# Performance work log

Measured on AMD Instinct MI355X. Metric: run time of the kernel, lower is better.

The kernel has to match this reference:

```python
import jax, jax.numpy as jnp
import numpy as np

B, C, L = 16, 128, 2048


def setup_inputs() -> dict:
    key = jax.random.key(0)
    ks = jax.random.split(key, 7)
    s = 1.0 / np.sqrt(C)  # torch Conv1d default init scale
    x = jax.random.normal(ks[0], (B, C, L), dtype=jnp.float32)
    W1 = jax.random.uniform(ks[1], (C, C), jnp.float32, -s, s)
    b1 = jax.random.uniform(ks[2], (C,), jnp.float32, -s, s)
    W2 = jax.random.uniform(ks[3], (C, C), jnp.float32, -s, s)
    b2 = jax.random.uniform(ks[4], (C,), jnp.float32, -s, s)
    W3 = jax.random.uniform(ks[5], (C, C), jnp.float32, -s, s)
    b3 = jax.random.uniform(ks[6], (C,), jnp.float32, -s, s)
    return {"x": x, "W1": W1, "b1": b1, "W2": W2, "b2": b2, "W3": W3, "b3": b3}


def _conv1x1(x, W, b):
    # x: [B,C,L], W: [out,in] -> [B,out,L]
    return jnp.einsum('oc,bcl->bol', W, x) + b[None, :, None]


def reference(x, W1, b1, W2, b2, W3, b3):
    q = _conv1x1(x, W1, b1).transpose(0, 2, 1)  # [B,L,C]
    k = _conv1x1(x, W2, b2).transpose(0, 2, 1)  # [B,L,C]
    v = _conv1x1(x, W3, b3).transpose(0, 2, 1)  # [B,L,C]
    attn = jnp.einsum('bic,bjc->bij', q, k)     # [B,L,L]
    attn = jax.nn.softmax(attn, axis=-1)
    out = jnp.einsum('bij,bjc->bic', attn, v)   # [B,L,C]
    return out.transpose(0, 2, 1)               # [B,C,L]
```

## Files before the change

kernel.cpp:

```cpp
#include <hip/hip_runtime.h>
#include <hip/hip_bf16.h>
#include <stdint.h>

#define B_ 16
#define C_ 128
#define L_ 2048
#define LOG2E 1.4426950408889634f

typedef __attribute__((ext_vector_type(8))) short bf16x8;
typedef __attribute__((ext_vector_type(4))) float f32x4;

typedef __attribute__((address_space(3))) unsigned int lds_u32_t;
typedef const __attribute__((address_space(1))) unsigned int gbl_u32_t;

__device__ __forceinline__ void gload_lds16(const void* g, void* l) {
  __builtin_amdgcn_global_load_lds((gbl_u32_t*)g,
                                   (lds_u32_t*)(unsigned long long)l, 16, 0, 0);
}

__device__ __forceinline__ unsigned short f2bf(float x) {
  union { float f; unsigned u; } v; v.f = x;
  unsigned u = v.u;
  u += 0x7fffu + ((u >> 16) & 1u);
  return (unsigned short)(u >> 16);
}

__device__ __forceinline__ unsigned pk2(float a, float b) {
  return (unsigned)f2bf(a) | ((unsigned)f2bf(b) << 16);
}

__global__ __launch_bounds__(256, 2) void proj_kernel(
    const float* __restrict__ x,
    const float* __restrict__ W1, const float* __restrict__ b1,
    const float* __restrict__ W2, const float* __restrict__ b2,
    const float* __restrict__ W3, const float* __restrict__ b3,
    unsigned short* __restrict__ Qo, unsigned short* __restrict__ Ko,
    unsigned short* __restrict__ Vt)
{
  __shared__ unsigned short Xt[64][136];
  __shared__ unsigned short Wl[128][136];

  const int b  = blockIdx.x & 15;
  const int lt = blockIdx.x >> 4;
  const int l0 = lt * 64;
  const int tid = threadIdx.x;
  const int w = tid >> 6, lane = tid & 63, li = lane & 15, lg = lane >> 4;

  for (int it = 0; it < 8; ++it) {
    int idx = tid + it * 256;
    int c = idx >> 4, f4 = idx & 15;
    const float4 vv = *(const float4*)(x + (size_t)(b * C_ + c) * L_ + l0 + f4 * 4);
    Xt[f4 * 4 + 0][c] = f2bf(vv.x);
    Xt[f4 * 4 + 1][c] = f2bf(vv.y);
    Xt[f4 * 4 + 2][c] = f2bf(vv.z);
    Xt[f4 * 4 + 3][c] = f2bf(vv.w);
  }

  auto stageW = [&](const float* W) {
    for (int it = 0; it < 16; ++it) {
      int idx = tid + it * 256;
      int o = idx >> 5, f4 = idx & 31;
      const float4 vv = *(const float4*)(W + (size_t)o * C_ + f4 * 4);
      unsigned short* p = &Wl[o][f4 * 4];
      p[0] = f2bf(vv.x); p[1] = f2bf(vv.y); p[2] = f2bf(vv.z); p[3] = f2bf(vv.w);
    }
  };

  auto computePhase = [&](const float* bias, unsigned short* Out, int mode) {
    f32x4 acc[8];
#pragma unroll
    for (int ni = 0; ni < 8; ++ni) acc[ni] = (f32x4){0.f, 0.f, 0.f, 0.f};
    bf16x8 af[4];
#pragma unroll
    for (int kk = 0; kk < 4; ++kk)
      af[kk] = *(const bf16x8*)&Xt[w * 16 + li][lg * 8 + kk * 32];
#pragma unroll
    for (int kk = 0; kk < 4; ++kk) {
#pragma unroll
      for (int ni = 0; ni < 8; ++ni) {
        bf16x8 bf = *(const bf16x8*)&Wl[ni * 16 + li][lg * 8 + kk * 32];
        acc[ni] = __builtin_amdgcn_mfma_f32_16x16x32_bf16(af[kk], bf, acc[ni], 0, 0, 0);
      }
    }
    if (mode == 0) {
#pragma unroll
      for (int ni = 0; ni < 8; ++ni) {
        float bv = bias[ni * 16 + li];
#pragma unroll
        for (int r = 0; r < 4; ++r) {
          int lrow = l0 + w * 16 + lg * 4 + r;
          Out[(size_t)(b * L_ + lrow) * C_ + ni * 16 + li] = f2bf(acc[ni][r] + bv);
        }
      }
    } else {
#pragma unroll
      for (int ni = 0; ni < 8; ++ni) {
        float bv = bias[ni * 16 + li];
        int o = ni * 16 + li;
        unsigned long long pw =
            (unsigned long long)pk2(acc[ni][0] + bv, acc[ni][1] + bv) |
            ((unsigned long long)pk2(acc[ni][2] + bv, acc[ni][3] + bv) << 32);
        *(unsigned long long*)(Out + (size_t)(b * C_ + o) * L_ + l0 + w * 16 + lg * 4) = pw;
      }
    }
  };

  stageW(W1);
  __syncthreads();
  computePhase(b1, Qo, 0);
  __syncthreads();
  stageW(W2);
  __syncthreads();
  computePhase(b2, Ko, 0);
  __syncthreads();
  stageW(W3);
  __syncthreads();
  computePhase(b3, Vt, 1);
}

__global__ __launch_bounds__(512, 2) void attn_kernel(
    const unsigned short* __restrict__ Q,
    const unsigned short* __restrict__ K,
    const unsigned short* __restrict__ Vt,
    float* __restrict__ out)
{
  __shared__ unsigned short kbuf[2][64 * C_];
  __shared__ unsigned short vbuf[2][C_ * 64];
  __shared__ unsigned short pbuf[8][16 * 64];

  const int b  = blockIdx.x & 15;
  const int qt = blockIdx.x >> 4;
  const int tid = threadIdx.x;
  const int w = tid >> 6, lane = tid & 63, li = lane & 15, lg = lane >> 4;
  const int qrow0 = qt * 128 + w * 16;
  const size_t bLC = (size_t)b * L_ * C_;

  bf16x8 qf[4];
  {
    const unsigned short* qp = Q + bLC + (size_t)(qrow0 + li) * C_ + lg * 8;
#pragma unroll
    for (int kk = 0; kk < 4; ++kk) qf[kk] = *(const bf16x8*)(qp + kk * 32);
  }

  f32x4 oacc[8];
#pragma unroll
  for (int i = 0; i < 8; ++i) oacc[i] = (f32x4){0.f, 0.f, 0.f, 0.f};
  float mrun = -1e30f, lrun = 0.f;

  const char* kgb = (const char*)(K + bLC);
  const char* vgb = (const char*)(Vt + bLC);

  auto stage = [&](int sel, int t) {
    const char* kt  = kgb + (size_t)t * (64 * 256);
    const char* vt0 = vgb + (size_t)t * 128;
    int dbase = w * 2048;
#pragma unroll
    for (int i2 = 0; i2 < 2; ++i2) {
      int db = dbase + i2 * 1024;
      int d  = db + lane * 16;
      int row = d >> 8, cb = d & 255;
      gload_lds16(kt + row * 256 + (cb ^ ((row & 7) << 4)), (char*)kbuf[sel] + db);
      int rowv = d >> 7, cbv = d & 127;
      gload_lds16(vt0 + (size_t)rowv * (L_ * 2) + (cbv ^ ((rowv & 7) << 4)),
                  (char*)vbuf[sel] + db);
    }
  };

  stage(0, 0);
  __syncthreads();

  int cur = 0;
  for (int t = 0; t < 32; ++t) {
    if (t + 1 < 32) stage(cur ^ 1, t + 1);

    const char* kb = (const char*)kbuf[cur];
    bf16x8 kf[4][4];
#pragma unroll
    for (int mt = 0; mt < 4; ++mt) {
      int row = mt * 16 + li;
      int rb = row << 8, swz = (row & 7) << 4;
#pragma unroll
      for (int kk = 0; kk < 4; ++kk)
        kf[mt][kk] = *(const bf16x8*)(kb + rb + ((lg * 16 + kk * 64) ^ swz));
    }
    f32x4 s[4];
#pragma unroll
    for (int mt = 0; mt < 4; ++mt) {
      s[mt] = (f32x4){0.f, 0.f, 0.f, 0.f};
#pragma unroll
      for (int kk = 0; kk < 4; ++kk)
        s[mt] = __builtin_amdgcn_mfma_f32_16x16x32_bf16(kf[mt][kk], qf[kk], s[mt], 0, 0, 0);
    }

    float pmax = -1e30f;
#pragma unroll
    for (int mt = 0; mt < 4; ++mt)
#pragma unroll
      for (int r = 0; r < 4; ++r) pmax = fmaxf(pmax, s[mt][r]);
    pmax = fmaxf(pmax, __shfl_xor(pmax, 16));
    pmax = fmaxf(pmax, __shfl_xor(pmax, 32));
    float mnew  = fmaxf(mrun, pmax);
    float alpha = exp2f((mrun - mnew) * LOG2E);
    float psum = 0.f;
#pragma unroll
    for (int mt = 0; mt < 4; ++mt) {
      float p0 = exp2f((s[mt][0] - mnew) * LOG2E);
      float p1 = exp2f((s[mt][1] - mnew) * LOG2E);
      float p2 = exp2f((s[mt][2] - mnew) * LOG2E);
      float p3 = exp2f((s[mt][3] - mnew) * LOG2E);
      psum += (p0 + p1) + (p2 + p3);
      unsigned long long pw = (unsigned long long)pk2(p0, p1) |
                              ((unsigned long long)pk2(p2, p3) << 32);
      int cb = mt * 32 + lg * 8;
      *(unsigned long long*)((char*)pbuf[w] + li * 128 + (cb ^ ((li & 7) << 4))) = pw;
    }
    psum += __shfl_xor(psum, 16);
    psum += __shfl_xor(psum, 32);
    lrun = lrun * alpha + psum;
#pragma unroll
    for (int ct = 0; ct < 8; ++ct) oacc[ct] = oacc[ct] * alpha;
    mrun = mnew;

    bf16x8 pf[2];
#pragma unroll
    for (int kk2 = 0; kk2 < 2; ++kk2)
      pf[kk2] = *(const bf16x8*)((const char*)pbuf[w] + li * 128 +
                                 ((lg * 16 + kk2 * 64) ^ ((li & 7) << 4)));
    const char* vb = (const char*)vbuf[cur];
#pragma unroll
    for (int ct = 0; ct < 8; ++ct) {
      int row = ct * 16 + li;
      int rb = row << 7, swz = (row & 7) << 4;
#pragma unroll
      for (int kk2 = 0; kk2 < 2; ++kk2) {
        bf16x8 vf = *(const bf16x8*)(vb + rb + ((lg * 16 + kk2 * 64) ^ swz));
        oacc[ct] = __builtin_amdgcn_mfma_f32_16x16x32_bf16(vf, pf[kk2], oacc[ct], 0, 0, 0);
      }
    }
    __syncthreads();
    cur ^= 1;
  }

  float inv = 1.0f / lrun;
  float* ob = out + (size_t)b * C_ * L_;
  int lcol = qt * 128 + w * 16 + li;
#pragma unroll
  for (int ct = 0; ct < 8; ++ct) {
    int c = ct * 16 + lg * 4;
#pragma unroll
    for (int r = 0; r < 4; ++r)
      ob[(size_t)(c + r) * L_ + lcol] = oacc[ct][r] * inv;
  }
}

extern "C" void kernel_launch(void* const* d_in, const int* in_sizes, int n_in,
                              void* d_out, int out_size, void* d_ws, size_t ws_size,
                              hipStream_t stream) {
  (void)in_sizes; (void)n_in; (void)out_size; (void)ws_size;
  const float* x  = (const float*)d_in[0];
  const float* W1 = (const float*)d_in[1];
  const float* b1 = (const float*)d_in[2];
  const float* W2 = (const float*)d_in[3];
  const float* b2 = (const float*)d_in[4];
  const float* W3 = (const float*)d_in[5];
  const float* b3 = (const float*)d_in[6];

  unsigned short* Q  = (unsigned short*)d_ws;
  unsigned short* K  = Q + (size_t)B_ * L_ * C_;
  unsigned short* Vt = K + (size_t)B_ * L_ * C_;

  proj_kernel<<<512, 256, 0, stream>>>(x, W1, b1, W2, b2, W3, b3, Q, K, Vt);
  attn_kernel<<<256, 512, 0, stream>>>(Q, K, Vt, (float*)d_out);
}
```

Before: 80.77 us.

## Rework attention to 32x32 MFMA with register-resident P and lazy rescale

The attention kernel moves from 16x16x32 to 32x32x16 bf16 MFMA, with each wave handling 32 query rows and the block shrunk to 4 waves. The softmax probabilities stay in registers, exchanged across lane halves with shuffles, instead of going through an LDS buffer. LOG2E is folded into Q in the projection kernel, the rescale of the running max is skipped unless it grows by more than 8, and packing uses the hardware bf16 convert instruction. Together these cut LDS traffic, VALU exp work and instruction count. The cost is fewer waves per block and higher register pressure.

```diff
diff --git a/kernel.cpp b/kernel.cpp
--- a/kernel.cpp
+++ b/kernel.cpp
@@ -9,6 +9,8 @@
 
 typedef __attribute__((ext_vector_type(8))) short bf16x8;
 typedef __attribute__((ext_vector_type(4))) float f32x4;
+typedef __attribute__((ext_vector_type(16))) float f32x16;
+typedef __attribute__((ext_vector_type(4))) unsigned int u32x4;
 
 typedef __attribute__((address_space(3))) unsigned int lds_u32_t;
 typedef const __attribute__((address_space(1))) unsigned int gbl_u32_t;
@@ -27,6 +29,38 @@
 
 __device__ __forceinline__ unsigned pk2(float a, float b) {
   return (unsigned)f2bf(a) | ((unsigned)f2bf(b) << 16);
+}
+
+__device__ __forceinline__ unsigned cvtpk_bf16(float lo, float hi_) {
+  unsigned r;
+  asm("v_cvt_pk_bf16_f32 %0, %1, %2" : "=v"(r) : "v"(lo), "v"(hi_));
+  return r;
+}
+
+__device__ __forceinline__ f32x16 z16() {
+  f32x16 v;
+#pragma unroll
+  for (int i = 0; i < 16; ++i) v[i] = 0.f;
+  return v;
+}
+
+__device__ __forceinline__ float tmax16(f32x16 v) {
+  float a0 = fmaxf(v[0], v[1]),  a1 = fmaxf(v[2], v[3]);
+  float a2 = fmaxf(v[4], v[5]),  a3 = fmaxf(v[6], v[7]);
+  float a4 = fmaxf(v[8], v[9]),  a5 = fmaxf(v[10], v[11]);
+  float a6 = fmaxf(v[12], v[13]), a7 = fmaxf(v[14], v[15]);
+  float b0 = fmaxf(a0, a1), b1 = fmaxf(a2, a3);
+  float b2 = fmaxf(a4, a5), b3 = fmaxf(a6, a7);
+  return fmaxf(fmaxf(b0, b1), fmaxf(b2, b3));
+}
+
+__device__ __forceinline__ float tsum16(f32x16 v) {
+  float a0 = v[0] + v[1],  a1 = v[2] + v[3];
+  float a2 = v[4] + v[5],  a3 = v[6] + v[7];
+  float a4 = v[8] + v[9],  a5 = v[10] + v[11];
+  float a6 = v[12] + v[13], a7 = v[14] + v[15];
+  float b0 = a0 + a1, b1 = a2 + a3, b2 = a4 + a5, b3 = a6 + a7;
+  return (b0 + b1) + (b2 + b3);
 }
 
 __global__ __launch_bounds__(256, 2) void proj_kernel(
@@ -66,7 +100,7 @@
     }
   };
 
-  auto computePhase = [&](const float* bias, unsigned short* Out, int mode) {
+  auto computePhase = [&](const float* bias, unsigned short* Out, int mode, float sc) {
     f32x4 acc[8];
 #pragma unroll
     for (int ni = 0; ni < 8; ++ni) acc[ni] = (f32x4){0.f, 0.f, 0.f, 0.f};
@@ -89,7 +123,7 @@
 #pragma unroll
         for (int r = 0; r < 4; ++r) {
           int lrow = l0 + w * 16 + lg * 4 + r;
-          Out[(size_t)(b * L_ + lrow) * C_ + ni * 16 + li] = f2bf(acc[ni][r] + bv);
+          Out[(size_t)(b * L_ + lrow) * C_ + ni * 16 + li] = f2bf((acc[ni][r] + bv) * sc);
         }
       }
     } else {
@@ -107,18 +141,18 @@
 
   stageW(W1);
   __syncthreads();
-  computePhase(b1, Qo, 0);
+  computePhase(b1, Qo, 0, LOG2E);
   __syncthreads();
   stageW(W2);
   __syncthreads();
-  computePhase(b2, Ko, 0);
+  computePhase(b2, Ko, 0, 1.0f);
   __syncthreads();
   stageW(W3);
   __syncthreads();
-  computePhase(b3, Vt, 1);
-}
-
-__global__ __launch_bounds__(512, 2) void attn_kernel(
+  computePhase(b3, Vt, 1, 1.0f);
+}
+
+__global__ __launch_bounds__(256, 1) void attn_kernel(
     const unsigned short* __restrict__ Q,
     const unsigned short* __restrict__ K,
     const unsigned short* __restrict__ Vt,
@@ -126,42 +160,41 @@
 {
   __shared__ unsigned short kbuf[2][64 * C_];
   __shared__ unsigned short vbuf[2][C_ * 64];
-  __shared__ unsigned short pbuf[8][16 * 64];
 
   const int b  = blockIdx.x & 15;
   const int qt = blockIdx.x >> 4;
   const int tid = threadIdx.x;
-  const int w = tid >> 6, lane = tid & 63, li = lane & 15, lg = lane >> 4;
-  const int qrow0 = qt * 128 + w * 16;
+  const int w = tid >> 6, lane = tid & 63;
+  const int q32 = lane & 31, hi = lane >> 5;
+  const int qrow = qt * 128 + w * 32 + q32;
   const size_t bLC = (size_t)b * L_ * C_;
 
-  bf16x8 qf[4];
+  bf16x8 qf[8];
   {
-    const unsigned short* qp = Q + bLC + (size_t)(qrow0 + li) * C_ + lg * 8;
-#pragma unroll
-    for (int kk = 0; kk < 4; ++kk) qf[kk] = *(const bf16x8*)(qp + kk * 32);
+    const unsigned short* qp = Q + bLC + (size_t)qrow * C_ + hi * 8;
+#pragma unroll
+    for (int kt = 0; kt < 8; ++kt) qf[kt] = *(const bf16x8*)(qp + kt * 16);
   }
 
-  f32x4 oacc[8];
-#pragma unroll
-  for (int i = 0; i < 8; ++i) oacc[i] = (f32x4){0.f, 0.f, 0.f, 0.f};
-  float mrun = -1e30f, lrun = 0.f;
+  f32x16 oacc[4];
+#pragma unroll
+  for (int i = 0; i < 4; ++i) oacc[i] = z16();
+  float m2 = -3e38f, lrun = 0.f;
 
   const char* kgb = (const char*)(K + bLC);
   const char* vgb = (const char*)(Vt + bLC);
 
   auto stage = [&](int sel, int t) {
-    const char* kt  = kgb + (size_t)t * (64 * 256);
+    const char* ktb = kgb + (size_t)t * (64 * 256);
     const char* vt0 = vgb + (size_t)t * 128;
-    int dbase = w * 2048;
-#pragma unroll
-    for (int i2 = 0; i2 < 2; ++i2) {
-      int db = dbase + i2 * 1024;
+#pragma unroll
+    for (int i2 = 0; i2 < 4; ++i2) {
+      int db = w * 4096 + i2 * 1024;
       int d  = db + lane * 16;
       int row = d >> 8, cb = d & 255;
-      gload_lds16(kt + row * 256 + (cb ^ ((row & 7) << 4)), (char*)kbuf[sel] + db);
-      int rowv = d >> 7, cbv = d & 127;
-      gload_lds16(vt0 + (size_t)rowv * (L_ * 2) + (cbv ^ ((rowv & 7) << 4)),
+      gload_lds16(ktb + row * 256 + (cb ^ ((row & 7) << 4)), (char*)kbuf[sel] + db);
+      int rc = d >> 7, cv = d & 127;
+      gload_lds16(vt0 + (size_t)rc * (L_ * 2) + (cv ^ ((rc & 7) << 4)),
                   (char*)vbuf[sel] + db);
     }
   };
@@ -174,82 +207,80 @@
     if (t + 1 < 32) stage(cur ^ 1, t + 1);
 
     const char* kb = (const char*)kbuf[cur];
-    bf16x8 kf[4][4];
-#pragma unroll
-    for (int mt = 0; mt < 4; ++mt) {
-      int row = mt * 16 + li;
-      int rb = row << 8, swz = (row & 7) << 4;
-#pragma unroll
-      for (int kk = 0; kk < 4; ++kk)
-        kf[mt][kk] = *(const bf16x8*)(kb + rb + ((lg * 16 + kk * 64) ^ swz));
-    }
-    f32x4 s[4];
-#pragma unroll
-    for (int mt = 0; mt < 4; ++mt) {
-      s[mt] = (f32x4){0.f, 0.f, 0.f, 0.f};
-#pragma unroll
-      for (int kk = 0; kk < 4; ++kk)
-        s[mt] = __builtin_amdgcn_mfma_f32_16x16x32_bf16(kf[mt][kk], qf[kk], s[mt], 0, 0, 0);
-    }
-
-    float pmax = -1e30f;
-#pragma unroll
-    for (int mt = 0; mt < 4; ++mt)
-#pragma unroll
-      for (int r = 0; r < 4; ++r) pmax = fmaxf(pmax, s[mt][r]);
-    pmax = fmaxf(pmax, __shfl_xor(pmax, 16));
-    pmax = fmaxf(pmax, __shfl_xor(pmax, 32));
-    float mnew  = fmaxf(mrun, pmax);
-    float alpha = exp2f((mrun - mnew) * LOG2E);
-    float psum = 0.f;
-#pragma unroll
-    for (int mt = 0; mt < 4; ++mt) {
-      float p0 = exp2f((s[mt][0] - mnew) * LOG2E);
-      float p1 = exp2f((s[mt][1] - mnew) * LOG2E);
-      float p2 = exp2f((s[mt][2] - mnew) * LOG2E);
-      float p3 = exp2f((s[mt][3] - mnew) * LOG2E);
-      psum += (p0 + p1) + (p2 + p3);
-      unsigned long long pw = (unsigned long long)pk2(p0, p1) |
-                              ((unsigned long long)pk2(p2, p3) << 32);
-      int cb = mt * 32 + lg * 8;
-      *(unsigned long long*)((char*)pbuf[w] + li * 128 + (cb ^ ((li & 7) << 4))) = pw;
-    }
-    psum += __shfl_xor(psum, 16);
-    psum += __shfl_xor(psum, 32);
-    lrun = lrun * alpha + psum;
-#pragma unroll
-    for (int ct = 0; ct < 8; ++ct) oacc[ct] = oacc[ct] * alpha;
-    mrun = mnew;
-
-    bf16x8 pf[2];
-#pragma unroll
-    for (int kk2 = 0; kk2 < 2; ++kk2)
-      pf[kk2] = *(const bf16x8*)((const char*)pbuf[w] + li * 128 +
-                                 ((lg * 16 + kk2 * 64) ^ ((li & 7) << 4)));
+    f32x16 s0 = z16(), s1 = z16();
+#pragma unroll
+    for (int kt2 = 0; kt2 < 8; ++kt2) {
+      int row0 = q32, row1 = 32 + q32;
+      bf16x8 kf0 = *(const bf16x8*)(kb + (row0 << 8) +
+                                    ((kt2 * 32 + hi * 16) ^ ((row0 & 7) << 4)));
+      bf16x8 kf1 = *(const bf16x8*)(kb + (row1 << 8) +
+                                    ((kt2 * 32 + hi * 16) ^ ((row1 & 7) << 4)));
+      s0 = __builtin_amdgcn_mfma_f32_32x32x16_bf16(kf0, qf[kt2], s0, 0, 0, 0);
+      s1 = __builtin_amdgcn_mfma_f32_32x32x16_bf16(kf1, qf[kt2], s1, 0, 0, 0);
+    }
+
+    float pm = fmaxf(tmax16(s0), tmax16(s1));
+    pm = fmaxf(pm, __shfl_xor(pm, 32));
+    if (!__all(pm - m2 <= 8.f)) {
+      float mn = fmaxf(m2, pm);
+      float al = exp2f(m2 - mn);
+      lrun *= al;
+#pragma unroll
+      for (int ct = 0; ct < 4; ++ct) oacc[ct] = oacc[ct] * al;
+      m2 = mn;
+    }
+#pragma unroll
+    for (int r = 0; r < 16; ++r) {
+      s0[r] = exp2f(s0[r] - m2);
+      s1[r] = exp2f(s1[r] - m2);
+    }
+    float ps = tsum16(s0) + tsum16(s1);
+    ps += __shfl_xor(ps, 32);
+    lrun += ps;
+
     const char* vb = (const char*)vbuf[cur];
-#pragma unroll
-    for (int ct = 0; ct < 8; ++ct) {
-      int row = ct * 16 + li;
-      int rb = row << 7, swz = (row & 7) << 4;
-#pragma unroll
-      for (int kk2 = 0; kk2 < 2; ++kk2) {
-        bf16x8 vf = *(const bf16x8*)(vb + rb + ((lg * 16 + kk2 * 64) ^ swz));
-        oacc[ct] = __builtin_amdgcn_mfma_f32_16x16x32_bf16(vf, pf[kk2], oacc[ct], 0, 0, 0);
+    auto pvstep = [&](const f32x16& sv, int kj) {
+      const int base = (kj & 1) * 8;
+      unsigned wl0 = cvtpk_bf16(sv[base + 0], sv[base + 1]);
+      unsigned wl1 = cvtpk_bf16(sv[base + 2], sv[base + 3]);
+      unsigned wh0 = cvtpk_bf16(sv[base + 4], sv[base + 5]);
+      unsigned wh1 = cvtpk_bf16(sv[base + 6], sv[base + 7]);
+      unsigned snd0 = hi ? wl0 : wh0;
+      unsigned snd1 = hi ? wl1 : wh1;
+      unsigned rcv0 = (unsigned)__shfl_xor((int)snd0, 32);
+      unsigned rcv1 = (unsigned)__shfl_xor((int)snd1, 32);
+      unsigned w0 = hi ? rcv0 : wl0;
+      unsigned w1 = hi ? rcv1 : wl1;
+      unsigned w2 = hi ? wh0 : rcv0;
+      unsigned w3 = hi ? wh1 : rcv1;
+      u32x4 pw = {w0, w1, w2, w3};
+      bf16x8 pf = *reinterpret_cast<bf16x8*>(&pw);
+#pragma unroll
+      for (int ct = 0; ct < 4; ++ct) {
+        int rowc = ct * 32 + q32;
+        bf16x8 vf = *(const bf16x8*)(vb + (rowc << 7) +
+                                     ((kj * 32 + hi * 16) ^ ((rowc & 7) << 4)));
+        oacc[ct] = __builtin_amdgcn_mfma_f32_32x32x16_bf16(vf, pf, oacc[ct], 0, 0, 0);
       }
-    }
+    };
+    pvstep(s0, 0);
+    pvstep(s0, 1);
+    pvstep(s1, 2);
+    pvstep(s1, 3);
+
     __syncthreads();
     cur ^= 1;
   }
 
   float inv = 1.0f / lrun;
-  float* ob = out + (size_t)b * C_ * L_;
-  int lcol = qt * 128 + w * 16 + li;
-#pragma unroll
-  for (int ct = 0; ct < 8; ++ct) {
-    int c = ct * 16 + lg * 4;
-#pragma unroll
-    for (int r = 0; r < 4; ++r)
-      ob[(size_t)(c + r) * L_ + lcol] = oacc[ct][r] * inv;
+  float* ob = out + (size_t)b * C_ * L_ + qrow;
+#pragma unroll
+  for (int ct = 0; ct < 4; ++ct) {
+#pragma unroll
+    for (int r = 0; r < 16; ++r) {
+      int c = ct * 32 + (r & 3) + 8 * (r >> 2) + 4 * hi;
+      ob[(size_t)c * L_] = oacc[ct][r] * inv;
+    }
   }
 }
 
@@ -270,5 +301,5 @@
   unsigned short* Vt = K + (size_t)B_ * L_ * C_;
 
   proj_kernel<<<512, 256, 0, stream>>>(x, W1, b1, W2, b2, W3, b3, Q, K, Vt);
-  attn_kernel<<<256, 512, 0, stream>>>(Q, K, Vt, (float*)d_out);
-}
+  attn_kernel<<<256, 256, 0, stream>>>(Q, K, Vt, (float*)d_out);
+}
```

New measurement: 85.97 us. 6.4% more time.
